# Kernel tuning notes

Measured on AMD Instinct MI355X. Metric: run time of the kernel, lower is better.

## Reference

```python
import jax, jax.numpy as jnp
import numpy as np

NUM_EXPERTS = 8
DIM = 2048
BATCH = 8192


def setup_inputs() -> dict:
    key = jax.random.key(0)
    k_x, k_ids, k_w, k_b = jax.random.split(key, 4)
    x = jax.random.normal(k_x, (BATCH, DIM), dtype=jnp.float32)
    cam_pred_ids = jax.random.randint(k_ids, (BATCH,), 0, NUM_EXPERTS, dtype=jnp.int64)
    # torch nn.Linear default init: U(-1/sqrt(in), 1/sqrt(in)); W is [out, in]
    bound = 1.0 / np.sqrt(DIM)
    W = jax.random.uniform(k_w, (NUM_EXPERTS, DIM, DIM), dtype=jnp.float32,
                           minval=-bound, maxval=bound)
    b = jax.random.uniform(k_b, (NUM_EXPERTS, DIM), dtype=jnp.float32,
                           minval=-bound, maxval=bound)
    return {"x": x, "cam_pred_ids": cam_pred_ids, "W": W, "b": b}


def reference(x, cam_pred_ids, W, b):
    # Per-sample expert routing: out[i] = x[i] + relu(x[i] @ W[e].T + b[e]),
    # where e = cam_pred_ids[i]. Vectorized as 8 full-batch GEMMs with masked
    # combine (fixed small expert count -> Python loop is structural, not data).
    h = jnp.zeros_like(x)
    for e in range(NUM_EXPERTS):
        he = jax.nn.relu(x @ W[e].T + b[e])          # [B, D]
        mask = (cam_pred_ids == e)[:, None]
        h = h + jnp.where(mask, he, jnp.zeros((), dtype=x.dtype))
    return x + h
```

## Files before the change

### kernel.cpp

```cpp
#include <hip/hip_runtime.h>
#include <hip/hip_bf16.h>
#include <stdint.h>

#define BATCH 8192
#define DIM   2048
#define NEXP  8
#define BM    128
#define BN    128
#define BK    32
#define NITER (DIM / BK)
#define MAX_TILES 72
#define NBLK  (DIM / BN)
#define NROWS 9216
#define XROWB 2304
#define WCVTB 2048

typedef __bf16 bf16x8 __attribute__((ext_vector_type(8)));
typedef float  f32x4  __attribute__((ext_vector_type(4)));

#define XG_BYTE_OFF 40960ull
#define WB_BYTE_OFF 37789696ull
#define WS_NEED     104898560ull

#define AS1(p) ((const __attribute__((address_space(1))) void*)(p))
#define AS3(p) ((__attribute__((address_space(3))) void*)(p))

__device__ __forceinline__ unsigned f2bf2(float lo, float hi) {
    unsigned ul = __float_as_uint(lo), uh = __float_as_uint(hi);
    ul = (ul + 0x7FFFu + ((ul >> 16) & 1u)) >> 16;
    uh = (uh + 0x7FFFu + ((uh >> 16) & 1u)) >> 16;
    return (uh << 16) | ul;
}

__global__ __launch_bounds__(512)
void k_plan(const int* __restrict__ ids, int* __restrict__ ws,
            int* __restrict__ rowmap) {
    __shared__ int sc[512 * NEXP];
    __shared__ int seg[NEXP];
    __shared__ int tot[NEXP];
    int t = threadIdx.x;
    int myids[16];
    int base = t * 16;
#pragma unroll
    for (int e = 0; e < NEXP; e++) sc[t * NEXP + e] = 0;
#pragma unroll
    for (int i = 0; i < 16; i++) {
        myids[i] = ids[base + i];
        sc[t * NEXP + myids[i]]++;
    }
    __syncthreads();
    {
        int w = t >> 6, l = t & 63;
        int e = w;
        int vals[8], sum = 0;
#pragma unroll
        for (int j = 0; j < 8; j++) { vals[j] = sc[(l * 8 + j) * NEXP + e]; sum += vals[j]; }
        int inc = sum;
        for (int d = 1; d < 64; d <<= 1) {
            int v = __shfl_up(inc, d, 64);
            if (l >= d) inc += v;
        }
        int run = inc - sum;
#pragma unroll
        for (int j = 0; j < 8; j++) { int v = vals[j]; sc[(l * 8 + j) * NEXP + e] = run; run += v; }
        if (l == 63) tot[e] = run;
    }
    __syncthreads();
    if (t == 0) {
        int pos = 0, mt = 0;
        for (int e = 0; e < NEXP; e++) {
            int c = tot[e];
            seg[e] = pos;
            int ntl = (c + BM - 1) / BM;
            for (int tt = 0; tt < ntl; tt++) {
                ws[64  + mt] = e;
                ws[160 + mt] = pos + tt * BM;
                int v = c - tt * BM;
                ws[256 + mt] = v < BM ? v : BM;
                mt++;
            }
            pos += ntl * BM;
        }
        ws[48] = mt;
    }
    __syncthreads();
    for (int i = t; i < NROWS; i += 512) rowmap[i] = -1;
    __syncthreads();
#pragma unroll
    for (int i = 0; i < 16; i++) {
        int e = myids[i];
        int p = seg[e] + sc[t * NEXP + e]++;
        rowmap[p] = base + i;
    }
}

__global__ __launch_bounds__(512)
void k_prep(const float* __restrict__ x, const int* __restrict__ rowmap,
            unsigned short* __restrict__ xg,
            const float4* __restrict__ W, uint4* __restrict__ Wb) {
    int b = blockIdx.x;
    int t = threadIdx.x;
    if (b < XROWB) {
        int rm[4];
#pragma unroll
        for (int r = 0; r < 4; r++) rm[r] = rowmap[b * 4 + r];
#pragma unroll
        for (int r = 0; r < 4; r++) {
            int row = b * 4 + r;
            uint2* o = (uint2*)(xg + (size_t)row * DIM);
            if (rm[r] < 0) { o[t] = make_uint2(0, 0); continue; }
            float4 a = ((const float4*)(x + (size_t)rm[r] * DIM))[t];
            uint2 v;
            v.x = f2bf2(a.x, a.y);
            v.y = f2bf2(a.z, a.w);
            o[t] = v;
        }
        return;
    }
    size_t base = (size_t)(b - XROWB) * 2048;
#pragma unroll
    for (int j = 0; j < 4; j++) {
        size_t o = base + (size_t)j * 512 + t;
        float4 a = W[o * 2], c = W[o * 2 + 1];
        uint4 v;
        v.x = f2bf2(a.x, a.y);  v.y = f2bf2(a.z, a.w);
        v.z = f2bf2(c.x, c.y);  v.w = f2bf2(c.z, c.w);
        Wb[o] = v;
    }
}

__launch_bounds__(256)
__global__ void k_gemm(const unsigned short* __restrict__ xg,
                       const unsigned short* __restrict__ Wb,
                       const float* __restrict__ bias,
                       const int* __restrict__ ws, const int* __restrict__ rowmap,
                       float* __restrict__ out) {
    int mt = blockIdx.y;
    if (mt >= ws[48]) return;
    int e     = ws[64  + mt];
    int pos0  = ws[160 + mt];
    int valid = ws[256 + mt];
    int n0 = blockIdx.x * BN;

    __shared__ unsigned short lds[2][8192];

    int tid = threadIdx.x;
    int w = tid >> 6, l = tid & 63;
    int lane15 = l & 15, quad = l >> 4;
    int wave_m = (w >> 1) * 64, wave_n = (w & 1) * 64;

    const unsigned short* Abase = xg + (size_t)pos0 * DIM;
    const unsigned short* Bbase = Wb + (size_t)e * DIM * DIM + (size_t)n0 * DIM;

    int srcOff[2];
#pragma unroll
    for (int j = 0; j < 2; j++) {
        int c = w * 128 + j * 64 + l;
        int row = c >> 2, pos = c & 3;
        int q = pos ^ ((row >> 1) & 3);
        srcOff[j] = row * DIM + q * 8;
    }

    int swz = (quad ^ ((lane15 >> 1) & 3)) * 8;
    int afOff[4], bfOff[4];
#pragma unroll
    for (int mi = 0; mi < 4; mi++)
        afOff[mi] = (wave_m + mi * 16 + lane15) * BK + swz;
#pragma unroll
    for (int ni = 0; ni < 4; ni++)
        bfOff[ni] = 4096 + (wave_n + ni * 16 + lane15) * BK + swz;

    f32x4 acc[4][4];
#pragma unroll
    for (int i = 0; i < 4; i++)
#pragma unroll
        for (int j = 0; j < 4; j++) acc[i][j] = (f32x4){0.f, 0.f, 0.f, 0.f};

#define ISSUE(buf, k0)                                                          \
    do {                                                                        \
        _Pragma("unroll")                                                       \
        for (int j = 0; j < 2; j++) {                                           \
            __builtin_amdgcn_global_load_lds(                                   \
                AS1(Abase + (k0) + srcOff[j]),                                  \
                AS3(&lds[buf][w * 1024 + j * 512]), 16, 0, 0);                  \
            __builtin_amdgcn_global_load_lds(                                   \
                AS1(Bbase + (k0) + srcOff[j]),                                  \
                AS3(&lds[buf][4096 + w * 1024 + j * 512]), 16, 0, 0);           \
        }                                                                       \
    } while (0)

    ISSUE(0, 0);
    int cur = 0;
    for (int i = 0; i < NITER; ++i) {
        __syncthreads();
        if (i + 1 < NITER) {
            int k0n = (i + 1) * BK;
            ISSUE(cur ^ 1, k0n);
        }
        bf16x8 af[4], bf[4];
#pragma unroll
        for (int mi = 0; mi < 4; mi++)
            af[mi] = *(const bf16x8*)(&lds[cur][afOff[mi]]);
#pragma unroll
        for (int ni = 0; ni < 4; ni++)
            bf[ni] = *(const bf16x8*)(&lds[cur][bfOff[ni]]);
#pragma unroll
        for (int mi = 0; mi < 4; mi++)
#pragma unroll
            for (int ni = 0; ni < 4; ni++)
                acc[mi][ni] = __builtin_amdgcn_mfma_f32_16x16x32_bf16(
                    af[mi], bf[ni], acc[mi][ni], 0, 0, 0);
        cur ^= 1;
    }
#undef ISSUE

    float bv[4];
#pragma unroll
    for (int ni = 0; ni < 4; ni++)
        bv[ni] = bias[(size_t)e * DIM + n0 + wave_n + ni * 16 + lane15];
#pragma unroll
    for (int mi = 0; mi < 4; mi++) {
#pragma unroll
        for (int r4 = 0; r4 < 4; r4++) {
            int rl = wave_m + mi * 16 + quad * 4 + r4;
            if (rl < valid) {
                int orig = rowmap[pos0 + rl];
                const unsigned short* xrow = xg + (size_t)(pos0 + rl) * DIM + n0;
                float* orow = out + (size_t)orig * DIM + n0;
#pragma unroll
                for (int ni = 0; ni < 4; ni++) {
                    int col = wave_n + ni * 16 + lane15;
                    float xv = __uint_as_float((unsigned)xrow[col] << 16);
                    float v = acc[mi][ni][r4] + bv[ni];
                    v = v > 0.f ? v : 0.f;
                    orow[col] = xv + v;
                }
            }
        }
    }
}

__global__ void k_naive(const float* __restrict__ x, const int* __restrict__ ids,
                        const float* __restrict__ W, const float* __restrict__ b,
                        float* __restrict__ out) {
    __shared__ float lx[DIM];
    int i = blockIdx.x;
    for (int t = threadIdx.x; t < DIM; t += blockDim.x) lx[t] = x[(size_t)i * DIM + t];
    __syncthreads();
    int e = ids[i];
    const float* We = W + (size_t)e * DIM * DIM;
    for (int n = threadIdx.x; n < DIM; n += blockDim.x) {
        const float* wr = We + (size_t)n * DIM;
        float acc = 0.f;
        for (int k = 0; k < DIM; k += 4) {
            float4 w4 = *(const float4*)(wr + k);
            acc += lx[k] * w4.x + lx[k + 1] * w4.y + lx[k + 2] * w4.z + lx[k + 3] * w4.w;
        }
        float v = acc + b[(size_t)e * DIM + n];
        v = v > 0.f ? v : 0.f;
        out[(size_t)i * DIM + n] = lx[n] + v;
    }
}

extern "C" void kernel_launch(void* const* d_in, const int* in_sizes, int n_in,
                              void* d_out, int out_size, void* d_ws, size_t ws_size,
                              hipStream_t stream) {
    const float* x   = (const float*)d_in[0];
    const int*   ids = (const int*)d_in[1];
    const float* W   = (const float*)d_in[2];
    const float* b   = (const float*)d_in[3];
    float* out = (float*)d_out;

    if (ws_size < WS_NEED) {
        k_naive<<<BATCH, 256, 0, stream>>>(x, ids, W, b, out);
        return;
    }

    char* wsb = (char*)d_ws;
    int*  wsi = (int*)wsb;
    int* rowmap = wsi + 512;
    unsigned short* xg = (unsigned short*)(wsb + XG_BYTE_OFF);
    unsigned short* Wb = (unsigned short*)(wsb + WB_BYTE_OFF);

    k_plan<<<1, 512, 0, stream>>>(ids, wsi, rowmap);
    k_prep<<<XROWB + WCVTB, 512, 0, stream>>>(x, rowmap, xg,
                                              (const float4*)W, (uint4*)Wb);
    dim3 g(NBLK, MAX_TILES);
    k_gemm<<<g, 256, 0, stream>>>(xg, Wb, b, wsi, rowmap, out);
}
```

Baseline: 396.9 us.

## Fuse weight fp32-to-bf16 conversion into GEMM by loading fp32 W tiles to LDS

Drops the separate pass that converts all expert weights to bf16 in workspace. The GEMM now streams fp32 weight tiles straight into LDS with a swizzled layout and converts them to bf16 in registers before the MFMA. This removes a full read and write of the 128MB weight tensor, but doubles B-tile global traffic and LDS footprint inside the GEMM. Each weight tile is re-read by up to 72 row tiles, and the conversion now runs again on every pass, adding ALU work in the inner loop.

```diff
diff --git a/kernel.cpp b/kernel.cpp
--- a/kernel.cpp
+++ b/kernel.cpp
@@ -13,14 +13,12 @@
 #define NBLK  (DIM / BN)
 #define NROWS 9216
 #define XROWB 2304
-#define WCVTB 2048
 
 typedef __bf16 bf16x8 __attribute__((ext_vector_type(8)));
 typedef float  f32x4  __attribute__((ext_vector_type(4)));
 
 #define XG_BYTE_OFF 40960ull
-#define WB_BYTE_OFF 37789696ull
-#define WS_NEED     104898560ull
+#define WS_NEED     37789696ull
 
 #define AS1(p) ((const __attribute__((address_space(1))) void*)(p))
 #define AS3(p) ((__attribute__((address_space(3))) void*)(p))
@@ -96,42 +94,28 @@
 
 __global__ __launch_bounds__(512)
 void k_prep(const float* __restrict__ x, const int* __restrict__ rowmap,
-            unsigned short* __restrict__ xg,
-            const float4* __restrict__ W, uint4* __restrict__ Wb) {
+            unsigned short* __restrict__ xg) {
     int b = blockIdx.x;
     int t = threadIdx.x;
-    if (b < XROWB) {
-        int rm[4];
-#pragma unroll
-        for (int r = 0; r < 4; r++) rm[r] = rowmap[b * 4 + r];
-#pragma unroll
-        for (int r = 0; r < 4; r++) {
-            int row = b * 4 + r;
-            uint2* o = (uint2*)(xg + (size_t)row * DIM);
-            if (rm[r] < 0) { o[t] = make_uint2(0, 0); continue; }
-            float4 a = ((const float4*)(x + (size_t)rm[r] * DIM))[t];
-            uint2 v;
-            v.x = f2bf2(a.x, a.y);
-            v.y = f2bf2(a.z, a.w);
-            o[t] = v;
-        }
-        return;
-    }
-    size_t base = (size_t)(b - XROWB) * 2048;
-#pragma unroll
-    for (int j = 0; j < 4; j++) {
-        size_t o = base + (size_t)j * 512 + t;
-        float4 a = W[o * 2], c = W[o * 2 + 1];
-        uint4 v;
-        v.x = f2bf2(a.x, a.y);  v.y = f2bf2(a.z, a.w);
-        v.z = f2bf2(c.x, c.y);  v.w = f2bf2(c.z, c.w);
-        Wb[o] = v;
+    int rm[4];
+#pragma unroll
+    for (int r = 0; r < 4; r++) rm[r] = rowmap[b * 4 + r];
+#pragma unroll
+    for (int r = 0; r < 4; r++) {
+        int row = b * 4 + r;
+        uint2* o = (uint2*)(xg + (size_t)row * DIM);
+        if (rm[r] < 0) { o[t] = make_uint2(0, 0); continue; }
+        float4 a = ((const float4*)(x + (size_t)rm[r] * DIM))[t];
+        uint2 v;
+        v.x = f2bf2(a.x, a.y);
+        v.y = f2bf2(a.z, a.w);
+        o[t] = v;
     }
 }
 
 __launch_bounds__(256)
 __global__ void k_gemm(const unsigned short* __restrict__ xg,
-                       const unsigned short* __restrict__ Wb,
+                       const float* __restrict__ W,
                        const float* __restrict__ bias,
                        const int* __restrict__ ws, const int* __restrict__ rowmap,
                        float* __restrict__ out) {
@@ -142,7 +126,7 @@
     int valid = ws[256 + mt];
     int n0 = blockIdx.x * BN;
 
-    __shared__ unsigned short lds[2][8192];
+    __shared__ unsigned char lds[2][24576];
 
     int tid = threadIdx.x;
     int w = tid >> 6, l = tid & 63;
@@ -150,25 +134,38 @@
     int wave_m = (w >> 1) * 64, wave_n = (w & 1) * 64;
 
     const unsigned short* Abase = xg + (size_t)pos0 * DIM;
-    const unsigned short* Bbase = Wb + (size_t)e * DIM * DIM + (size_t)n0 * DIM;
-
-    int srcOff[2];
+    const float* Bbase = W + ((size_t)e * DIM + n0) * DIM;
+
+    int srcA[2];
 #pragma unroll
     for (int j = 0; j < 2; j++) {
         int c = w * 128 + j * 64 + l;
         int row = c >> 2, pos = c & 3;
         int q = pos ^ ((row >> 1) & 3);
-        srcOff[j] = row * DIM + q * 8;
-    }
-
-    int swz = (quad ^ ((lane15 >> 1) & 3)) * 8;
-    int afOff[4], bfOff[4];
+        srcA[j] = row * DIM + q * 8;
+    }
+    int srcB[4];
+#pragma unroll
+    for (int j = 0; j < 4; j++) {
+        int c = w * 256 + j * 64 + l;
+        int row = c >> 3, pos = c & 7;
+        int q = pos ^ (row & 7);
+        srcB[j] = row * DIM + q * 4;
+    }
+
+    int aswz = (quad ^ ((lane15 >> 1) & 3)) * 16;
+    int afOff[4];
 #pragma unroll
     for (int mi = 0; mi < 4; mi++)
-        afOff[mi] = (wave_m + mi * 16 + lane15) * BK + swz;
-#pragma unroll
-    for (int ni = 0; ni < 4; ni++)
-        bfOff[ni] = 4096 + (wave_n + ni * 16 + lane15) * BK + swz;
+        afOff[mi] = (wave_m + mi * 16 + lane15) * (BK * 2) + aswz;
+    int b0Off[4], b1Off[4];
+#pragma unroll
+    for (int ni = 0; ni < 4; ni++) {
+        int r = wave_n + ni * 16 + lane15;
+        int s = r & 7;
+        b0Off[ni] = 8192 + r * 128 + ((quad * 2)     ^ s) * 16;
+        b1Off[ni] = 8192 + r * 128 + ((quad * 2 + 1) ^ s) * 16;
+    }
 
     f32x4 acc[4][4];
 #pragma unroll
@@ -176,17 +173,18 @@
 #pragma unroll
         for (int j = 0; j < 4; j++) acc[i][j] = (f32x4){0.f, 0.f, 0.f, 0.f};
 
-#define ISSUE(buf, k0)                                                          \
-    do {                                                                        \
-        _Pragma("unroll")                                                       \
-        for (int j = 0; j < 2; j++) {                                           \
-            __builtin_amdgcn_global_load_lds(                                   \
-                AS1(Abase + (k0) + srcOff[j]),                                  \
-                AS3(&lds[buf][w * 1024 + j * 512]), 16, 0, 0);                  \
-            __builtin_amdgcn_global_load_lds(                                   \
-                AS1(Bbase + (k0) + srcOff[j]),                                  \
-                AS3(&lds[buf][4096 + w * 1024 + j * 512]), 16, 0, 0);           \
-        }                                                                       \
+#define ISSUE(buf, k0)                                                         \
+    do {                                                                       \
+        _Pragma("unroll")                                                      \
+        for (int j = 0; j < 2; j++)                                            \
+            __builtin_amdgcn_global_load_lds(                                  \
+                AS1(Abase + (k0) + srcA[j]),                                   \
+                AS3(&lds[buf][w * 2048 + j * 1024]), 16, 0, 0);                \
+        _Pragma("unroll")                                                      \
+        for (int j = 0; j < 4; j++)                                            \
+            __builtin_amdgcn_global_load_lds(                                  \
+                AS1(Bbase + (k0) + srcB[j]),                                   \
+                AS3(&lds[buf][8192 + w * 4096 + j * 1024]), 16, 0, 0);         \
     } while (0)
 
     ISSUE(0, 0);
@@ -202,8 +200,16 @@
         for (int mi = 0; mi < 4; mi++)
             af[mi] = *(const bf16x8*)(&lds[cur][afOff[mi]]);
 #pragma unroll
-        for (int ni = 0; ni < 4; ni++)
-            bf[ni] = *(const bf16x8*)(&lds[cur][bfOff[ni]]);
+        for (int ni = 0; ni < 4; ni++) {
+            float4 u = *(const float4*)(&lds[cur][b0Off[ni]]);
+            float4 v = *(const float4*)(&lds[cur][b1Off[ni]]);
+            bf16x8 tbf;
+            tbf[0] = (__bf16)u.x; tbf[1] = (__bf16)u.y;
+            tbf[2] = (__bf16)u.z; tbf[3] = (__bf16)u.w;
+            tbf[4] = (__bf16)v.x; tbf[5] = (__bf16)v.y;
+            tbf[6] = (__bf16)v.z; tbf[7] = (__bf16)v.w;
+            bf[ni] = tbf;
+        }
 #pragma unroll
         for (int mi = 0; mi < 4; mi++)
 #pragma unroll
@@ -280,11 +286,9 @@
     int*  wsi = (int*)wsb;
     int* rowmap = wsi + 512;
     unsigned short* xg = (unsigned short*)(wsb + XG_BYTE_OFF);
-    unsigned short* Wb = (unsigned short*)(wsb + WB_BYTE_OFF);
 
     k_plan<<<1, 512, 0, stream>>>(ids, wsi, rowmap);
-    k_prep<<<XROWB + WCVTB, 512, 0, stream>>>(x, rowmap, xg,
-                                              (const float4*)W, (uint4*)Wb);
+    k_prep<<<XROWB, 512, 0, stream>>>(x, rowmap, xg);
     dim3 g(NBLK, MAX_TILES);
-    k_gemm<<<g, 256, 0, stream>>>(xg, Wb, b, wsi, rowmap, out);
-}
+    k_gemm<<<g, 256, 0, stream>>>(xg, W, b, wsi, rowmap, out);
+}
```

Result: slower. 419.5 us (+5.7%).
